# Kernel tuning notes

Hardware: AMD Instinct MI355X
Metric: run time of the kernel (lower is better)

Reference implementation:

```python
import jax, jax.numpy as jnp
import numpy as np

N = 50000
E = 1600000
D = 128
NUM_BOND_FEATS = 3
BOND_VOCAB = 5
BN_EPS = 1e-5


def setup_inputs() -> dict:
    key = jax.random.key(0)
    ks = jax.random.split(key, 12)
    x = jax.random.normal(ks[0], (N, D), dtype=jnp.float32)
    edge_attr = jax.random.randint(ks[1], (E, NUM_BOND_FEATS), 0, BOND_VOCAB, dtype=jnp.int64)
    src = jax.random.randint(ks[2], (E,), 0, N, dtype=jnp.int64)
    dst = jax.random.randint(ks[3], (E,), 0, N, dtype=jnp.int64)
    # BondEncoder: one embedding table per bond feature
    bond_emb = jax.random.normal(ks[4], (NUM_BOND_FEATS, BOND_VOCAB, D), dtype=jnp.float32) * 0.02
    # GIN eps parameter (init 0)
    eps = jnp.zeros((), dtype=jnp.float32)
    # MLP: Linear(D,D) -> BatchNorm1d(D) -> ReLU -> Linear(D,D)
    s = 1.0 / np.sqrt(D)
    W1 = jax.random.uniform(ks[5], (D, D), minval=-s, maxval=s, dtype=jnp.float32)
    b1 = jax.random.uniform(ks[6], (D,), minval=-s, maxval=s, dtype=jnp.float32)
    gamma = jnp.ones((D,), dtype=jnp.float32)
    beta = jnp.zeros((D,), dtype=jnp.float32)
    W2 = jax.random.uniform(ks[7], (D, D), minval=-s, maxval=s, dtype=jnp.float32)
    b2 = jax.random.uniform(ks[8], (D,), minval=-s, maxval=s, dtype=jnp.float32)
    return {"x": x, "edge_attr": edge_attr, "src": src, "dst": dst,
            "bond_emb": bond_emb, "eps": eps, "W1": W1, "b1": b1,
            "gamma": gamma, "beta": beta, "W2": W2, "b2": b2}


def reference(x, edge_attr, src, dst, bond_emb, eps, W1, b1, gamma, beta, W2, b2):
    # BondEncoder: sum of per-feature categorical embeddings -> [E, D]
    edge_embedding = bond_emb[jnp.arange(NUM_BOND_FEATS)[None, :], edge_attr].sum(axis=1)
    # copy_u gather + add edge emb + ReLU (per-edge messages)
    m = jax.nn.relu(x[src] + edge_embedding)            # [E, D]
    # scatter-sum aggregation to destination nodes
    agg = jax.ops.segment_sum(m, dst, num_segments=N)   # [N, D]
    h = (1.0 + eps) * x + agg
    # MLP: Linear -> BatchNorm (batch stats, training mode) -> ReLU -> Linear
    h1 = h @ W1 + b1
    mean = jnp.mean(h1, axis=0)
    var = jnp.var(h1, axis=0)
    hn = (h1 - mean) * jax.lax.rsqrt(var + BN_EPS) * gamma + beta
    out = jax.nn.relu(hn) @ W2 + b2
    return out
```

## Files before the change

kernel.cpp:

```cpp
#include <hip/hip_runtime.h>
#include <hip/hip_bf16.h>

#define NN 50000
#define NE 1600000
#define D 128
#define NB 784
#define CAP 2560
#define EPT 4

__device__ __forceinline__ void fma4(float4& acc, float s, const float4& w) {
  acc.x = fmaf(s, w.x, acc.x);
  acc.y = fmaf(s, w.y, acc.y);
  acc.z = fmaf(s, w.z, acc.z);
  acc.w = fmaf(s, w.w, acc.w);
}

__device__ __forceinline__ unsigned short f2bf(float f) {
  unsigned u = __float_as_uint(f);
  u += 0x7FFFu + ((u >> 16) & 1u);
  return (unsigned short)(u >> 16);
}
__device__ __forceinline__ float bf2f(unsigned short h) {
  return __uint_as_float((unsigned)h << 16);
}

__global__ __launch_bounds__(256) void k_half(const float* __restrict__ x,
                                              const float* __restrict__ bemb,
                                              ushort* __restrict__ xh,
                                              float* __restrict__ ctab) {
  const int gid = blockIdx.x * 256 + threadIdx.x;

  if (gid < 125 * D) {
    const int c = gid >> 7;
    const int k = gid & 127;
    ctab[gid] = bemb[(c / 25) * D + k] + bemb[(5 + (c % 25) / 5) * D + k] +
                bemb[(10 + c % 5) * D + k];
  }

  const int i4 = gid * 4;
  if (i4 < NN * D) {
    const float4 v = *(const float4*)(x + i4);
    ushort4 h;
    h.x = f2bf(v.x); h.y = f2bf(v.y); h.z = f2bf(v.z); h.w = f2bf(v.w);
    *(ushort4*)(xh + i4) = h;
  }
}

__global__ __launch_bounds__(1024) void k_bin(const int* __restrict__ dst,
                                              const int* __restrict__ src,
                                              const int* __restrict__ ea,
                                              int* __restrict__ bucketCnt,
                                              unsigned* __restrict__ staging) {
  __shared__ int lcnt[NB], gbase[NB], lcur[NB];
  const int tid = threadIdx.x;
  for (int i = tid; i < NB; i += 1024) { lcnt[i] = 0; lcur[i] = 0; }
  __syncthreads();

  const int gid = blockIdx.x * 1024 + tid;
  const int e0 = gid * EPT;
  const bool act = (e0 < NE);

  int d[EPT];
  unsigned rec[EPT];
  if (act) {
    const int4 dv = *(const int4*)(dst + e0);
    const int4 sv = *(const int4*)(src + e0);
    const int4* ap = (const int4*)(ea + 3 * e0);
    int a[12];
#pragma unroll
    for (int q = 0; q < 3; ++q) {
      const int4 v = ap[q];
      a[4 * q + 0] = v.x; a[4 * q + 1] = v.y; a[4 * q + 2] = v.z; a[4 * q + 3] = v.w;
    }
    d[0] = dv.x; d[1] = dv.y; d[2] = dv.z; d[3] = dv.w;
    rec[0] = sv.x; rec[1] = sv.y; rec[2] = sv.z; rec[3] = sv.w;
#pragma unroll
    for (int q = 0; q < EPT; ++q) {
      const unsigned cb = (unsigned)((a[3 * q] * 5 + a[3 * q + 1]) * 5 + a[3 * q + 2]);
      rec[q] |= (cb << 16) | ((unsigned)(d[q] & 63) << 23);
      atomicAdd(&lcnt[d[q] >> 6], 1);
    }
  }
  __syncthreads();
  for (int i = tid; i < NB; i += 1024)
    gbase[i] = atomicAdd(&bucketCnt[i], lcnt[i]);
  __syncthreads();
  if (act) {
#pragma unroll
    for (int q = 0; q < EPT; ++q) {
      const int b = d[q] >> 6;
      const int r = atomicAdd(&lcur[b], 1) + gbase[b];
      if (r < CAP) staging[(size_t)b * CAP + r] = rec[q];
    }
  }
}

__global__ __launch_bounds__(1024) void k_fine(const int* __restrict__ bucketCnt,
                                               unsigned* __restrict__ staging,
                                               int* __restrict__ beg,
                                               int* __restrict__ end) {
  __shared__ unsigned srec[CAP];
  __shared__ int hist[64], off[64], cur[64];
  const int tid = threadIdx.x;
  const int b = blockIdx.x;
  const int base = b * CAP;
  const int cnt = min(bucketCnt[b], CAP);

  if (tid < 64) { hist[tid] = 0; cur[tid] = 0; }
  for (int i = tid; i < cnt; i += 1024) srec[i] = staging[base + i];
  __syncthreads();
  for (int i = tid; i < cnt; i += 1024) atomicAdd(&hist[srec[i] >> 23], 1);
  __syncthreads();
  int v = 0;
  if (tid < 64) { v = hist[tid]; off[tid] = v; }
  __syncthreads();
  for (int s = 1; s < 64; s <<= 1) {
    int u = 0;
    if (tid < 64 && tid >= s) u = off[tid - s];
    __syncthreads();
    if (tid < 64) off[tid] += u;
    __syncthreads();
  }
  if (tid < 64) off[tid] -= v;
  __syncthreads();

  if (tid < 64) {
    const int n = b * 64 + tid;
    if (n < NN) {
      beg[n] = base + off[tid];
      end[n] = base + off[tid] + hist[tid];
    }
  }
  for (int i = tid; i < cnt; i += 1024) {
    const unsigned u = srec[i];
    const int node = u >> 23;
    const int r = atomicAdd(&cur[node], 1);
    staging[base + off[node] + r] = u & 0x7FFFFFu;
  }
}

__global__ __launch_bounds__(256, 4) void k_agg(const float* __restrict__ x,
                                                const ushort* __restrict__ xh,
                                                const float* __restrict__ ctab,
                                                const float* __restrict__ epsp,
                                                const int* __restrict__ beg,
                                                const int* __restrict__ end,
                                                const unsigned* __restrict__ packed2,
                                                float* __restrict__ hbuf) {
  const int lane = threadIdx.x & 31;
  const int n = blockIdx.x * 8 + (threadIdx.x >> 5);
  const int col = lane << 2;

  const int jb = beg[n];
  const int je = end[n];
  float4 acc = make_float4(0.f, 0.f, 0.f, 0.f);

  for (int j0 = jb; j0 < je; j0 += 32) {
    const int rem = min(32, je - j0);
    const int pk = (j0 + lane < je) ? (int)packed2[j0 + lane] : 0;
    int t = 0;
    for (; t + 8 <= rem; t += 8) {
      unsigned p[8];
#pragma unroll
      for (int i = 0; i < 8; ++i) p[i] = (unsigned)__shfl(pk, t + i, 32);
      ushort4 xs[8];
#pragma unroll
      for (int i = 0; i < 8; ++i)
        xs[i] = *(const ushort4*)(xh + (size_t)(p[i] & 0xFFFF) * D + col);
#pragma unroll
      for (int i = 0; i < 8; ++i) {
        const float4 ev = *(const float4*)(ctab + ((p[i] >> 16) & 0x7F) * D + col);
        acc.x += fmaxf(bf2f(xs[i].x) + ev.x, 0.f);
        acc.y += fmaxf(bf2f(xs[i].y) + ev.y, 0.f);
        acc.z += fmaxf(bf2f(xs[i].z) + ev.z, 0.f);
        acc.w += fmaxf(bf2f(xs[i].w) + ev.w, 0.f);
      }
    }
    for (; t < rem; ++t) {
      const unsigned p = (unsigned)__shfl(pk, t, 32);
      const ushort4 xv = *(const ushort4*)(xh + (size_t)(p & 0xFFFF) * D + col);
      const float4 ev = *(const float4*)(ctab + ((p >> 16) & 0x7F) * D + col);
      acc.x += fmaxf(bf2f(xv.x) + ev.x, 0.f);
      acc.y += fmaxf(bf2f(xv.y) + ev.y, 0.f);
      acc.z += fmaxf(bf2f(xv.z) + ev.z, 0.f);
      acc.w += fmaxf(bf2f(xv.w) + ev.w, 0.f);
    }
  }

  const float eps1 = 1.0f + epsp[0];
  const float4 xv = *(const float4*)(x + (size_t)n * D + col);
  acc.x += eps1 * xv.x;
  acc.y += eps1 * xv.y;
  acc.z += eps1 * xv.z;
  acc.w += eps1 * xv.w;
  *(float4*)(hbuf + (size_t)n * D + col) = acc;
}

__global__ __launch_bounds__(256, 2) void k_gemm1(const float* __restrict__ hbuf,
                                                  const float* __restrict__ W1,
                                                  const float* __restrict__ b1,
                                                  float* __restrict__ h1,
                                                  float* __restrict__ gsum,
                                                  float* __restrict__ gsumsq) {
  __shared__ float shT[64 * 64];
  __shared__ float sW[64 * 128];

  const int tid = threadIdx.x;
  const int row0 = blockIdx.x * 64;
  const int cg = tid & 31;
  const int rt = tid >> 5;
  const int cbase = cg * 4;
  const int rbase = rt * 8;

  float4 acc[8];
  const float4 bias = *(const float4*)(b1 + cbase);
#pragma unroll
  for (int r = 0; r < 8; ++r) acc[r] = bias;

  for (int kh = 0; kh < 2; ++kh) {
    __syncthreads();
    for (int i = tid; i < 1024; i += 256) {
      const int r = i & 63;
      const int kc = (i >> 6) << 2;
      const int gr = row0 + r;
      float4 v = make_float4(0.f, 0.f, 0.f, 0.f);
      if (gr < NN) v = *(const float4*)(hbuf + (size_t)gr * D + kh * 64 + kc);
      shT[(kc + 0) * 64 + r] = v.x;
      shT[(kc + 1) * 64 + r] = v.y;
      shT[(kc + 2) * 64 + r] = v.z;
      shT[(kc + 3) * 64 + r] = v.w;
    }
    for (int i = tid; i < 2048; i += 256) {
      const int k = i >> 5;
      const int c4 = (i & 31) << 2;
      *(float4*)(sW + k * 128 + c4) = *(const float4*)(W1 + (size_t)(kh * 64 + k) * D + c4);
    }
    __syncthreads();
    for (int k = 0; k < 64; ++k) {
      const float4 a_lo = *(const float4*)(shT + k * 64 + rbase);
      const float4 a_hi = *(const float4*)(shT + k * 64 + rbase + 4);
      const float4 w = *(const float4*)(sW + k * 128 + cbase);
      fma4(acc[0], a_lo.x, w); fma4(acc[1], a_lo.y, w);
      fma4(acc[2], a_lo.z, w); fma4(acc[3], a_lo.w, w);
      fma4(acc[4], a_hi.x, w); fma4(acc[5], a_hi.y, w);
      fma4(acc[6], a_hi.z, w); fma4(acc[7], a_hi.w, w);
    }
  }

  float4 cs = make_float4(0.f, 0.f, 0.f, 0.f);
  float4 cq = make_float4(0.f, 0.f, 0.f, 0.f);
#pragma unroll
  for (int r = 0; r < 8; ++r) {
    const int gr = row0 + rbase + r;
    if (gr < NN) {
      *(float4*)(h1 + (size_t)gr * D + cbase) = acc[r];
      cs.x += acc[r].x; cs.y += acc[r].y; cs.z += acc[r].z; cs.w += acc[r].w;
      cq.x += acc[r].x * acc[r].x; cq.y += acc[r].y * acc[r].y;
      cq.z += acc[r].z * acc[r].z; cq.w += acc[r].w * acc[r].w;
    }
  }
  __syncthreads();
  float* ssum = shT;
  float* ssq = shT + 128;
  if (tid < 128) { ssum[tid] = 0.f; ssq[tid] = 0.f; }
  __syncthreads();
  atomicAdd(&ssum[cbase + 0], cs.x);
  atomicAdd(&ssum[cbase + 1], cs.y);
  atomicAdd(&ssum[cbase + 2], cs.z);
  atomicAdd(&ssum[cbase + 3], cs.w);
  atomicAdd(&ssq[cbase + 0], cq.x);
  atomicAdd(&ssq[cbase + 1], cq.y);
  atomicAdd(&ssq[cbase + 2], cq.z);
  atomicAdd(&ssq[cbase + 3], cq.w);
  __syncthreads();
  if (tid < 128) {
    atomicAdd(&gsum[tid], ssum[tid]);
    atomicAdd(&gsumsq[tid], ssq[tid]);
  }
}

__global__ __launch_bounds__(256, 2) void k_gemm2(const float* __restrict__ hbuf,
                                                  const float* __restrict__ gsum,
                                                  const float* __restrict__ gsq,
                                                  const float* __restrict__ gamma,
                                                  const float* __restrict__ beta,
                                                  const float* __restrict__ W2,
                                                  const float* __restrict__ b2,
                                                  float* __restrict__ out) {
  __shared__ float shT[64 * 64];
  __shared__ float sW[64 * 128];

  const int tid = threadIdx.x;
  const int row0 = blockIdx.x * 64;
  const int cg = tid & 31;
  const int rt = tid >> 5;
  const int cbase = cg * 4;
  const int rbase = rt * 8;
  const float invN = 1.0f / (float)NN;

  float4 acc[8];
  const float4 bias = *(const float4*)(b2 + cbase);
#pragma unroll
  for (int r = 0; r < 8; ++r) acc[r] = bias;

  for (int kh = 0; kh < 2; ++kh) {
    __syncthreads();
    for (int i = tid; i < 1024; i += 256) {
      const int r = i & 63;
      const int kc = (i >> 6) << 2;
      const int gr = row0 + r;
      const int kk = kh * 64 + kc;
      const float4 gs = *(const float4*)(gsum + kk);
      const float4 gq = *(const float4*)(gsq + kk);
      const float4 gm = *(const float4*)(gamma + kk);
      const float4 bt = *(const float4*)(beta + kk);
      const float m0 = gs.x * invN, m1 = gs.y * invN, m2 = gs.z * invN, m3 = gs.w * invN;
      const float A0 = gm.x * rsqrtf(gq.x * invN - m0 * m0 + 1e-5f);
      const float A1 = gm.y * rsqrtf(gq.y * invN - m1 * m1 + 1e-5f);
      const float A2 = gm.z * rsqrtf(gq.z * invN - m2 * m2 + 1e-5f);
      const float A3 = gm.w * rsqrtf(gq.w * invN - m3 * m3 + 1e-5f);
      float4 v = make_float4(0.f, 0.f, 0.f, 0.f);
      if (gr < NN) {
        const float4 h = *(const float4*)(hbuf + (size_t)gr * D + kk);
        v.x = fmaxf(fmaf(h.x - m0, A0, bt.x), 0.f);
        v.y = fmaxf(fmaf(h.y - m1, A1, bt.y), 0.f);
        v.z = fmaxf(fmaf(h.z - m2, A2, bt.z), 0.f);
        v.w = fmaxf(fmaf(h.w - m3, A3, bt.w), 0.f);
      }
      shT[(kc + 0) * 64 + r] = v.x;
      shT[(kc + 1) * 64 + r] = v.y;
      shT[(kc + 2) * 64 + r] = v.z;
      shT[(kc + 3) * 64 + r] = v.w;
    }
    for (int i = tid; i < 2048; i += 256) {
      const int k = i >> 5;
      const int c4 = (i & 31) << 2;
      *(float4*)(sW + k * 128 + c4) = *(const float4*)(W2 + (size_t)(kh * 64 + k) * D + c4);
    }
    __syncthreads();
    for (int k = 0; k < 64; ++k) {
      const float4 a_lo = *(const float4*)(shT + k * 64 + rbase);
      const float4 a_hi = *(const float4*)(shT + k * 64 + rbase + 4);
      const float4 w = *(const float4*)(sW + k * 128 + cbase);
      fma4(acc[0], a_lo.x, w); fma4(acc[1], a_lo.y, w);
      fma4(acc[2], a_lo.z, w); fma4(acc[3], a_lo.w, w);
      fma4(acc[4], a_hi.x, w); fma4(acc[5], a_hi.y, w);
      fma4(acc[6], a_hi.z, w); fma4(acc[7], a_hi.w, w);
    }
  }

#pragma unroll
  for (int r = 0; r < 8; ++r) {
    const int gr = row0 + rbase + r;
    if (gr < NN) *(float4*)(out + (size_t)gr * D + cbase) = acc[r];
  }
}

extern "C" void kernel_launch(void* const* d_in, const int* in_sizes, int n_in,
                              void* d_out, int out_size, void* d_ws, size_t ws_size,
                              hipStream_t stream) {
  const float* x    = (const float*)d_in[0];
  const int* ea     = (const int*)d_in[1];
  const int* src    = (const int*)d_in[2];
  const int* dst    = (const int*)d_in[3];
  const float* bemb = (const float*)d_in[4];
  const float* epsp = (const float*)d_in[5];
  const float* W1   = (const float*)d_in[6];
  const float* b1   = (const float*)d_in[7];
  const float* gam  = (const float*)d_in[8];
  const float* bet  = (const float*)d_in[9];
  const float* W2   = (const float*)d_in[10];
  const float* b2   = (const float*)d_in[11];
  float* out = (float*)d_out;

  float* ws         = (float*)d_ws;
  float* hbuf       = ws;
  int* bucketCnt    = (int*)(ws + (size_t)NN * D);
  float* gsum       = ws + (size_t)NN * D + NB;
  float* gsumsq     = gsum + D;
  int* beg          = (int*)(gsumsq + D);
  int* endp         = beg + NN;
  float* ctab       = (float*)(endp + NN);
  ushort* xh        = (ushort*)(ctab + 125 * D);
  unsigned* staging = (unsigned*)(xh + (size_t)NN * D);

  hipMemsetAsync(bucketCnt, 0, (size_t)(NB + 2 * D) * sizeof(int), stream);

  k_half<<<(NN * D / 4 + 255) / 256, 256, 0, stream>>>(x, bemb, xh, ctab);
  k_bin<<<(NE / EPT + 1023) / 1024, 1024, 0, stream>>>(dst, src, ea, bucketCnt, staging);
  k_fine<<<NB, 1024, 0, stream>>>(bucketCnt, staging, beg, endp);
  k_agg<<<NN / 8, 256, 0, stream>>>(x, xh, ctab, epsp, beg, endp, staging, hbuf);
  k_gemm1<<<(NN + 63) / 64, 256, 0, stream>>>(hbuf, W1, b1, hbuf, gsum, gsumsq);
  k_gemm2<<<(NN + 63) / 64, 256, 0, stream>>>(hbuf, gsum, gsumsq, gam, bet, W2, b2, out);
}
```

Before: 311.9 us.

## Replace FP32 SIMT GEMMs with bf16 MFMA kernels using split-precision activations

Both dense 128x128 layers are rewritten to use MFMA 16x16x32 bf16 instructions instead of scalar FP32 FMAs on LDS-transposed tiles. The weights are transposed and converted to bf16 once in the prep kernel. The first GEMM splits each activation into hi and lo bf16 parts to keep accuracy before BatchNorm. The second folds BN into per-column scale and shift and uses a single bf16 pass. The row buffer is padded to a multiple of 64 and zeroed so tiles need no bounds checks on loads, at the cost of reduced precision and an extra memset.

```diff
diff --git a/kernel.cpp b/kernel.cpp
--- a/kernel.cpp
+++ b/kernel.cpp
@@ -7,13 +7,11 @@
 #define NB 784
 #define CAP 2560
 #define EPT 4
-
-__device__ __forceinline__ void fma4(float4& acc, float s, const float4& w) {
-  acc.x = fmaf(s, w.x, acc.x);
-  acc.y = fmaf(s, w.y, acc.y);
-  acc.z = fmaf(s, w.z, acc.z);
-  acc.w = fmaf(s, w.w, acc.w);
-}
+#define NROW 50048
+#define LDWU 68
+
+typedef __attribute__((ext_vector_type(8))) short bf16x8;
+typedef __attribute__((ext_vector_type(4))) float f32x4;
 
 __device__ __forceinline__ unsigned short f2bf(float f) {
   unsigned u = __float_as_uint(f);
@@ -26,8 +24,12 @@
 
 __global__ __launch_bounds__(256) void k_half(const float* __restrict__ x,
                                               const float* __restrict__ bemb,
+                                              const float* __restrict__ W1,
+                                              const float* __restrict__ W2,
                                               ushort* __restrict__ xh,
-                                              float* __restrict__ ctab) {
+                                              float* __restrict__ ctab,
+                                              ushort* __restrict__ w1t,
+                                              ushort* __restrict__ w2t) {
   const int gid = blockIdx.x * 256 + threadIdx.x;
 
   if (gid < 125 * D) {
@@ -35,6 +37,15 @@
     const int k = gid & 127;
     ctab[gid] = bemb[(c / 25) * D + k] + bemb[(5 + (c % 25) / 5) * D + k] +
                 bemb[(10 + c % 5) * D + k];
+  }
+
+  if (gid < 2 * 16384) {
+    const int m = gid >> 14;
+    const int idx = gid & 16383;
+    const int c = idx >> 7;
+    const int k = idx & 127;
+    const float w = m ? W2[k * 128 + c] : W1[k * 128 + c];
+    (m ? w2t : w1t)[idx] = f2bf(w);
   }
 
   const int i4 = gid * 4;
@@ -196,82 +207,74 @@
   *(float4*)(hbuf + (size_t)n * D + col) = acc;
 }
 
-__global__ __launch_bounds__(256, 2) void k_gemm1(const float* __restrict__ hbuf,
-                                                  const float* __restrict__ W1,
+__global__ __launch_bounds__(256, 4) void k_mfma1(const float* __restrict__ hbuf,
+                                                  const ushort* __restrict__ w1t,
                                                   const float* __restrict__ b1,
                                                   float* __restrict__ h1,
                                                   float* __restrict__ gsum,
                                                   float* __restrict__ gsumsq) {
-  __shared__ float shT[64 * 64];
-  __shared__ float sW[64 * 128];
-
+  __shared__ uint sW[128 * LDWU];
+  __shared__ float ssum[128], ssq[128];
   const int tid = threadIdx.x;
-  const int row0 = blockIdx.x * 64;
-  const int cg = tid & 31;
-  const int rt = tid >> 5;
-  const int cbase = cg * 4;
-  const int rbase = rt * 8;
-
-  float4 acc[8];
-  const float4 bias = *(const float4*)(b1 + cbase);
-#pragma unroll
-  for (int r = 0; r < 8; ++r) acc[r] = bias;
-
-  for (int kh = 0; kh < 2; ++kh) {
-    __syncthreads();
-    for (int i = tid; i < 1024; i += 256) {
-      const int r = i & 63;
-      const int kc = (i >> 6) << 2;
-      const int gr = row0 + r;
-      float4 v = make_float4(0.f, 0.f, 0.f, 0.f);
-      if (gr < NN) v = *(const float4*)(hbuf + (size_t)gr * D + kh * 64 + kc);
-      shT[(kc + 0) * 64 + r] = v.x;
-      shT[(kc + 1) * 64 + r] = v.y;
-      shT[(kc + 2) * 64 + r] = v.z;
-      shT[(kc + 3) * 64 + r] = v.w;
-    }
-    for (int i = tid; i < 2048; i += 256) {
-      const int k = i >> 5;
-      const int c4 = (i & 31) << 2;
-      *(float4*)(sW + k * 128 + c4) = *(const float4*)(W1 + (size_t)(kh * 64 + k) * D + c4);
-    }
-    __syncthreads();
-    for (int k = 0; k < 64; ++k) {
-      const float4 a_lo = *(const float4*)(shT + k * 64 + rbase);
-      const float4 a_hi = *(const float4*)(shT + k * 64 + rbase + 4);
-      const float4 w = *(const float4*)(sW + k * 128 + cbase);
-      fma4(acc[0], a_lo.x, w); fma4(acc[1], a_lo.y, w);
-      fma4(acc[2], a_lo.z, w); fma4(acc[3], a_lo.w, w);
-      fma4(acc[4], a_hi.x, w); fma4(acc[5], a_hi.y, w);
-      fma4(acc[6], a_hi.z, w); fma4(acc[7], a_hi.w, w);
-    }
-  }
-
-  float4 cs = make_float4(0.f, 0.f, 0.f, 0.f);
-  float4 cq = make_float4(0.f, 0.f, 0.f, 0.f);
-#pragma unroll
-  for (int r = 0; r < 8; ++r) {
-    const int gr = row0 + rbase + r;
-    if (gr < NN) {
-      *(float4*)(h1 + (size_t)gr * D + cbase) = acc[r];
-      cs.x += acc[r].x; cs.y += acc[r].y; cs.z += acc[r].z; cs.w += acc[r].w;
-      cq.x += acc[r].x * acc[r].x; cq.y += acc[r].y * acc[r].y;
-      cq.z += acc[r].z * acc[r].z; cq.w += acc[r].w * acc[r].w;
-    }
-  }
-  __syncthreads();
-  float* ssum = shT;
-  float* ssq = shT + 128;
+  {
+    const uint* src = (const uint*)w1t;
+    for (int i = tid; i < 8192; i += 256)
+      sW[(i >> 6) * LDWU + (i & 63)] = src[i];
+  }
   if (tid < 128) { ssum[tid] = 0.f; ssq[tid] = 0.f; }
   __syncthreads();
-  atomicAdd(&ssum[cbase + 0], cs.x);
-  atomicAdd(&ssum[cbase + 1], cs.y);
-  atomicAdd(&ssum[cbase + 2], cs.z);
-  atomicAdd(&ssum[cbase + 3], cs.w);
-  atomicAdd(&ssq[cbase + 0], cq.x);
-  atomicAdd(&ssq[cbase + 1], cq.y);
-  atomicAdd(&ssq[cbase + 2], cq.z);
-  atomicAdd(&ssq[cbase + 3], cq.w);
+
+  const int l = tid & 63;
+  const int la = l & 15;
+  const int lb = l >> 4;
+  const int rowbase = blockIdx.x * 64 + (tid >> 6) * 16;
+  const int arow = rowbase + la;
+  const float* ap = hbuf + (size_t)arow * 128 + lb * 8;
+
+  f32x4 acc[8];
+#pragma unroll
+  for (int ct = 0; ct < 8; ++ct) acc[ct] = (f32x4){0.f, 0.f, 0.f, 0.f};
+
+#pragma unroll
+  for (int ks = 0; ks < 4; ++ks) {
+    const float4 a0 = *(const float4*)(ap + ks * 32);
+    const float4 a1 = *(const float4*)(ap + ks * 32 + 4);
+    const float af[8] = {a0.x, a0.y, a0.z, a0.w, a1.x, a1.y, a1.z, a1.w};
+    bf16x8 ahi, alo;
+#pragma unroll
+    for (int j = 0; j < 8; ++j) {
+      const unsigned short hh = f2bf(af[j]);
+      ahi[j] = (short)hh;
+      alo[j] = (short)f2bf(af[j] - bf2f(hh));
+    }
+#pragma unroll
+    for (int ct = 0; ct < 8; ++ct) {
+      const int c = ct * 16 + la;
+      const bf16x8 b = *(const bf16x8*)(sW + c * LDWU + ks * 16 + lb * 4);
+      acc[ct] = __builtin_amdgcn_mfma_f32_16x16x32_bf16(ahi, b, acc[ct], 0, 0, 0);
+      acc[ct] = __builtin_amdgcn_mfma_f32_16x16x32_bf16(alo, b, acc[ct], 0, 0, 0);
+    }
+  }
+
+#pragma unroll
+  for (int ct = 0; ct < 8; ++ct) {
+    const int col = ct * 16 + la;
+    const float bb = b1[col];
+    float s = 0.f, q = 0.f;
+#pragma unroll
+    for (int r = 0; r < 4; ++r) {
+      const int row = rowbase + lb * 4 + r;
+      if (row < NN) {
+        const float v = acc[ct][r] + bb;
+        h1[(size_t)row * 128 + col] = v;
+        s += v;
+        q += v * v;
+      }
+    }
+    s += __shfl_xor(s, 16, 64); q += __shfl_xor(q, 16, 64);
+    s += __shfl_xor(s, 32, 64); q += __shfl_xor(q, 32, 64);
+    if (lb == 0) { atomicAdd(&ssum[col], s); atomicAdd(&ssq[col], q); }
+  }
   __syncthreads();
   if (tid < 128) {
     atomicAdd(&gsum[tid], ssum[tid]);
@@ -279,80 +282,79 @@
   }
 }
 
-__global__ __launch_bounds__(256, 2) void k_gemm2(const float* __restrict__ hbuf,
+__global__ __launch_bounds__(256, 4) void k_mfma2(const float* __restrict__ h1,
+                                                  const ushort* __restrict__ w2t,
                                                   const float* __restrict__ gsum,
                                                   const float* __restrict__ gsq,
                                                   const float* __restrict__ gamma,
                                                   const float* __restrict__ beta,
-                                                  const float* __restrict__ W2,
                                                   const float* __restrict__ b2,
                                                   float* __restrict__ out) {
-  __shared__ float shT[64 * 64];
-  __shared__ float sW[64 * 128];
-
+  __shared__ uint sW[128 * LDWU];
+  __shared__ float bnA[128], bnB[128];
   const int tid = threadIdx.x;
-  const int row0 = blockIdx.x * 64;
-  const int cg = tid & 31;
-  const int rt = tid >> 5;
-  const int cbase = cg * 4;
-  const int rbase = rt * 8;
-  const float invN = 1.0f / (float)NN;
-
-  float4 acc[8];
-  const float4 bias = *(const float4*)(b2 + cbase);
-#pragma unroll
-  for (int r = 0; r < 8; ++r) acc[r] = bias;
-
-  for (int kh = 0; kh < 2; ++kh) {
-    __syncthreads();
-    for (int i = tid; i < 1024; i += 256) {
-      const int r = i & 63;
-      const int kc = (i >> 6) << 2;
-      const int gr = row0 + r;
-      const int kk = kh * 64 + kc;
-      const float4 gs = *(const float4*)(gsum + kk);
-      const float4 gq = *(const float4*)(gsq + kk);
-      const float4 gm = *(const float4*)(gamma + kk);
-      const float4 bt = *(const float4*)(beta + kk);
-      const float m0 = gs.x * invN, m1 = gs.y * invN, m2 = gs.z * invN, m3 = gs.w * invN;
-      const float A0 = gm.x * rsqrtf(gq.x * invN - m0 * m0 + 1e-5f);
-      const float A1 = gm.y * rsqrtf(gq.y * invN - m1 * m1 + 1e-5f);
-      const float A2 = gm.z * rsqrtf(gq.z * invN - m2 * m2 + 1e-5f);
-      const float A3 = gm.w * rsqrtf(gq.w * invN - m3 * m3 + 1e-5f);
-      float4 v = make_float4(0.f, 0.f, 0.f, 0.f);
-      if (gr < NN) {
-        const float4 h = *(const float4*)(hbuf + (size_t)gr * D + kk);
-        v.x = fmaxf(fmaf(h.x - m0, A0, bt.x), 0.f);
-        v.y = fmaxf(fmaf(h.y - m1, A1, bt.y), 0.f);
-        v.z = fmaxf(fmaf(h.z - m2, A2, bt.z), 0.f);
-        v.w = fmaxf(fmaf(h.w - m3, A3, bt.w), 0.f);
-      }
-      shT[(kc + 0) * 64 + r] = v.x;
-      shT[(kc + 1) * 64 + r] = v.y;
-      shT[(kc + 2) * 64 + r] = v.z;
-      shT[(kc + 3) * 64 + r] = v.w;
-    }
-    for (int i = tid; i < 2048; i += 256) {
-      const int k = i >> 5;
-      const int c4 = (i & 31) << 2;
-      *(float4*)(sW + k * 128 + c4) = *(const float4*)(W2 + (size_t)(kh * 64 + k) * D + c4);
-    }
-    __syncthreads();
-    for (int k = 0; k < 64; ++k) {
-      const float4 a_lo = *(const float4*)(shT + k * 64 + rbase);
-      const float4 a_hi = *(const float4*)(shT + k * 64 + rbase + 4);
-      const float4 w = *(const float4*)(sW + k * 128 + cbase);
-      fma4(acc[0], a_lo.x, w); fma4(acc[1], a_lo.y, w);
-      fma4(acc[2], a_lo.z, w); fma4(acc[3], a_lo.w, w);
-      fma4(acc[4], a_hi.x, w); fma4(acc[5], a_hi.y, w);
-      fma4(acc[6], a_hi.z, w); fma4(acc[7], a_hi.w, w);
-    }
-  }
-
-#pragma unroll
-  for (int r = 0; r < 8; ++r) {
-    const int gr = row0 + rbase + r;
-    if (gr < NN) *(float4*)(out + (size_t)gr * D + cbase) = acc[r];
+  {
+    const uint* src = (const uint*)w2t;
+    for (int i = tid; i < 8192; i += 256)
+      sW[(i >> 6) * LDWU + (i & 63)] = src[i];
+  }
+  if (tid < 128) {
+    const float invN = 1.0f / (float)NN;
+    const float m = gsum[tid] * invN;
+    const float A = gamma[tid] * rsqrtf(gsq[tid] * invN - m * m + 1e-5f);
+    bnA[tid] = A;
+    bnB[tid] = beta[tid] - m * A;
+  }
+  __syncthreads();
+
+  const int l = tid & 63;
+  const int la = l & 15;
+  const int lb = l >> 4;
+  const int rowbase = blockIdx.x * 64 + (tid >> 6) * 16;
+  const int arow = rowbase + la;
+  const float* ap = h1 + (size_t)arow * 128 + lb * 8;
+
+  f32x4 acc[8];
+#pragma unroll
+  for (int ct = 0; ct < 8; ++ct) acc[ct] = (f32x4){0.f, 0.f, 0.f, 0.f};
+
+#pragma unroll
+  for (int ks = 0; ks < 4; ++ks) {
+    const int k0 = ks * 32 + lb * 8;
+    const float4 a0 = *(const float4*)(ap + ks * 32);
+    const float4 a1 = *(const float4*)(ap + ks * 32 + 4);
+    const float4 cA0 = *(const float4*)(bnA + k0);
+    const float4 cA1 = *(const float4*)(bnA + k0 + 4);
+    const float4 cB0 = *(const float4*)(bnB + k0);
+    const float4 cB1 = *(const float4*)(bnB + k0 + 4);
+    const float af[8] = {fmaxf(fmaf(a0.x, cA0.x, cB0.x), 0.f),
+                         fmaxf(fmaf(a0.y, cA0.y, cB0.y), 0.f),
+                         fmaxf(fmaf(a0.z, cA0.z, cB0.z), 0.f),
+                         fmaxf(fmaf(a0.w, cA0.w, cB0.w), 0.f),
+                         fmaxf(fmaf(a1.x, cA1.x, cB1.x), 0.f),
+                         fmaxf(fmaf(a1.y, cA1.y, cB1.y), 0.f),
+                         fmaxf(fmaf(a1.z, cA1.z, cB1.z), 0.f),
+                         fmaxf(fmaf(a1.w, cA1.w, cB1.w), 0.f)};
+    bf16x8 afr;
+#pragma unroll
+    for (int j = 0; j < 8; ++j) afr[j] = (short)f2bf(af[j]);
+#pragma unroll
+    for (int ct = 0; ct < 8; ++ct) {
+      const int c = ct * 16 + la;
+      const bf16x8 b = *(const bf16x8*)(sW + c * LDWU + ks * 16 + lb * 4);
+      acc[ct] = __builtin_amdgcn_mfma_f32_16x16x32_bf16(afr, b, acc[ct], 0, 0, 0);
+    }
+  }
+
+#pragma unroll
+  for (int ct = 0; ct < 8; ++ct) {
+    const int col = ct * 16 + la;
+    const float bb = b2[col];
+#pragma unroll
+    for (int r = 0; r < 4; ++r) {
+      const int row = rowbase + lb * 4 + r;
+      if (row < NN) out[(size_t)row * 128 + col] = acc[ct][r] + bb;
+    }
   }
 }
 
@@ -375,21 +377,24 @@
 
   float* ws         = (float*)d_ws;
   float* hbuf       = ws;
-  int* bucketCnt    = (int*)(ws + (size_t)NN * D);
-  float* gsum       = ws + (size_t)NN * D + NB;
+  int* bucketCnt    = (int*)(ws + (size_t)NROW * D);
+  float* gsum       = ws + (size_t)NROW * D + NB;
   float* gsumsq     = gsum + D;
   int* beg          = (int*)(gsumsq + D);
   int* endp         = beg + NN;
   float* ctab       = (float*)(endp + NN);
-  ushort* xh        = (ushort*)(ctab + 125 * D);
+  ushort* w1t       = (ushort*)(ctab + 125 * D);
+  ushort* w2t       = w1t + 16384;
+  ushort* xh        = w2t + 16384;
   unsigned* staging = (unsigned*)(xh + (size_t)NN * D);
 
   hipMemsetAsync(bucketCnt, 0, (size_t)(NB + 2 * D) * sizeof(int), stream);
-
-  k_half<<<(NN * D / 4 + 255) / 256, 256, 0, stream>>>(x, bemb, xh, ctab);
+  hipMemsetAsync(hbuf + (size_t)NN * D, 0, (size_t)(NROW - NN) * D * sizeof(float), stream);
+
+  k_half<<<(NN * D / 4 + 255) / 256, 256, 0, stream>>>(x, bemb, W1, W2, xh, ctab, w1t, w2t);
   k_bin<<<(NE / EPT + 1023) / 1024, 1024, 0, stream>>>(dst, src, ea, bucketCnt, staging);
   k_fine<<<NB, 1024, 0, stream>>>(bucketCnt, staging, beg, endp);
   k_agg<<<NN / 8, 256, 0, stream>>>(x, xh, ctab, epsp, beg, endp, staging, hbuf);
-  k_gemm1<<<(NN + 63) / 64, 256, 0, stream>>>(hbuf, W1, b1, hbuf, gsum, gsumsq);
-  k_gemm2<<<(NN + 63) / 64, 256, 0, stream>>>(hbuf, gsum, gsumsq, gam, bet, W2, b2, out);
-}
+  k_mfma1<<<NROW / 64, 256, 0, stream>>>(hbuf, w1t, b1, hbuf, gsum, gsumsq);
+  k_mfma2<<<NROW / 64, 256, 0, stream>>>(hbuf, w2t, gsum, gsumsq, gam, bet, b2, out);
+}
```

Result: faster. 274.6 us (-12.0%).
